# Kernel optimization log

Hardware: AMD Instinct MI355X
Metric: run time of the kernel (lower is better)

## Reference

```python
import jax, jax.numpy as jnp
import numpy as np

HIDDEN = 2048
INTER = 1408
NUM_EXPERTS = 8
TOP_K = 2
BATCH, SEQ = 2, 1024


def setup_inputs() -> dict:
    key = jax.random.key(0)
    ks = jax.random.split(key, 8)
    s = 0.02
    return {
        "x": jax.random.normal(ks[0], (BATCH, SEQ, HIDDEN), dtype=jnp.float32),
        "router_w": jax.random.normal(ks[1], (NUM_EXPERTS, HIDDEN), dtype=jnp.float32) * s,
        "gate_w": jax.random.normal(ks[2], (NUM_EXPERTS, INTER, HIDDEN), dtype=jnp.float32) * s,
        "up_w": jax.random.normal(ks[3], (NUM_EXPERTS, INTER, HIDDEN), dtype=jnp.float32) * s,
        "down_w": jax.random.normal(ks[4], (NUM_EXPERTS, HIDDEN, INTER), dtype=jnp.float32) * s,
        "shared_gate_w": jax.random.normal(ks[5], (INTER, HIDDEN), dtype=jnp.float32) * s,
        "shared_up_w": jax.random.normal(ks[6], (INTER, HIDDEN), dtype=jnp.float32) * s,
        "shared_down_w": jax.random.normal(ks[7], (HIDDEN, INTER), dtype=jnp.float32) * s,
    }


def reference(x, router_w, gate_w, up_w, down_w,
              shared_gate_w, shared_up_w, shared_down_w):
    B, S, H = x.shape
    T = B * S
    E = router_w.shape[0]
    xf = x.reshape(T, H)

    # Router: softmax over experts, top-k selection, renormalized weights
    logits = xf @ router_w.T                       # [T, E]
    probs = jax.nn.softmax(logits, axis=-1)
    topw, topi = jax.lax.top_k(probs, TOP_K)       # [T, K]
    topw = topw / jnp.sum(topw, axis=-1, keepdims=True)

    # Combine weight per (token, expert): scatter-add of top-k weights
    comb = jnp.zeros((T, E), dtype=xf.dtype).at[
        jnp.arange(T)[:, None], topi].add(topw)    # [T, E]

    # All-expert SwiGLU (grouped GEMM form of masked gather/MLP/scatter)
    g = jnp.einsum('th,eih->tei', xf, gate_w)      # [T, E, I]
    u = jnp.einsum('th,eih->tei', xf, up_w)
    hmid = jax.nn.silu(g) * u
    eo = jnp.einsum('tei,ehi->teh', hmid, down_w)  # [T, E, H]
    out = jnp.einsum('te,teh->th', comb, eo)       # weighted combine

    # Shared expert applied to every token
    sh = (jax.nn.silu(xf @ shared_gate_w.T) * (xf @ shared_up_w.T)) @ shared_down_w.T
    out = out + sh
    return out.reshape(B, S, H)
```

## Files before the change

kernel.cpp:

```cpp
#include <hip/hip_runtime.h>
#include <cstdint>
#include <cstddef>

#define T_TOK 2048
#define HID   2048
#define INTER 1408
#define NEXP  8
#define NPAIR 6144
#define SLICE 2883584
#define BKS   32

#define NI1   22
#define GP1   24
#define NB1   (9 * GP1 * 16)
#define NI2   32
#define GP2   32
#define NB2   (9 * GP2 * 16)

typedef __bf16 bf16x8 __attribute__((ext_vector_type(8)));
typedef float  floatx4 __attribute__((ext_vector_type(4)));

static const size_t XB_OFF   = 0;
static const size_t HM_OFF   = XB_OFF + (size_t)T_TOK * HID * 2;
static const size_t GB_OFF   = HM_OFF + (size_t)NPAIR * INTER * 2;
static const size_t UB_OFF   = GB_OFF + (size_t)9 * SLICE * 2;
static const size_t DB_OFF   = UB_OFF + (size_t)9 * SLICE * 2;
static const size_t TOK_OFF  = DB_OFF + (size_t)9 * SLICE * 2;
static const size_t WGT_OFF  = TOK_OFF + (size_t)NPAIR * 4;
static const size_t TE_OFF   = WGT_OFF + (size_t)NPAIR * 4;
static const size_t TW_OFF   = TE_OFF + (size_t)T_TOK * 2 * 4;
static const size_t CTRL_OFF = TW_OFF + (size_t)T_TOK * 2 * 4;

static __device__ __forceinline__ unsigned short f2bf(float f) {
    unsigned u = __float_as_uint(f);
    u += 0x7fffu + ((u >> 16) & 1u);
    return (unsigned short)(u >> 16);
}
static __device__ __forceinline__ unsigned pk2(float a, float b) {
    return (unsigned)f2bf(a) | ((unsigned)f2bf(b) << 16);
}
static __device__ __forceinline__ void g2l16(const void* g, void* l) {
    __builtin_amdgcn_global_load_lds(
        (const __attribute__((address_space(1))) unsigned int*)g,
        (__attribute__((address_space(3))) unsigned int*)l, 16, 0, 0);
}

__global__ __launch_bounds__(256) void k_cvt_x(const float* __restrict__ x,
                                               unsigned short* __restrict__ xb) {
    int gid = blockIdx.x * 256 + threadIdx.x;
    const float4* src = (const float4*)x;
    float4 a = src[gid * 2], b = src[gid * 2 + 1];
    uint4 o;
    o.x = pk2(a.x, a.y); o.y = pk2(a.z, a.w);
    o.z = pk2(b.x, b.y); o.w = pk2(b.z, b.w);
    ((uint4*)xb)[gid] = o;
}

__global__ __launch_bounds__(256) void k_cvt_w(const float* __restrict__ g,
                                               const float* __restrict__ u,
                                               const float* __restrict__ d,
                                               const float* __restrict__ sg,
                                               const float* __restrict__ su,
                                               const float* __restrict__ sd,
                                               unsigned short* __restrict__ gb,
                                               unsigned short* __restrict__ ub,
                                               unsigned short* __restrict__ db) {
    int sl = blockIdx.z;
    const float* src;
    unsigned short* dst;
    if (blockIdx.y == 0) {
        src = (sl < 8) ? g + (size_t)sl * SLICE : sg;
        dst = gb + (size_t)sl * SLICE;
    } else if (blockIdx.y == 1) {
        src = (sl < 8) ? u + (size_t)sl * SLICE : su;
        dst = ub + (size_t)sl * SLICE;
    } else {
        src = (sl < 8) ? d + (size_t)sl * SLICE : sd;
        dst = db + (size_t)sl * SLICE;
    }
    int gid = blockIdx.x * 256 + threadIdx.x;
    const float4* s4 = (const float4*)src;
    float4 a = s4[gid * 2], b = s4[gid * 2 + 1];
    uint4 o;
    o.x = pk2(a.x, a.y); o.y = pk2(a.z, a.w);
    o.z = pk2(b.x, b.y); o.w = pk2(b.z, b.w);
    ((uint4*)dst)[gid] = o;
}

__global__ __launch_bounds__(256) void k_router(const float* __restrict__ x,
                                                const float* __restrict__ rw,
                                                int* __restrict__ te, float* __restrict__ tw,
                                                int* __restrict__ counts) {
    int wave = threadIdx.x >> 6, lane = threadIdx.x & 63;
    int t = blockIdx.x * 4 + wave;
    const float* xp = x + (size_t)t * HID;

    float acc[8];
#pragma unroll
    for (int e = 0; e < 8; ++e) acc[e] = 0.f;
    for (int i = lane; i < HID; i += 64) {
        float xv = xp[i];
#pragma unroll
        for (int e = 0; e < 8; ++e) acc[e] = fmaf(xv, rw[e * HID + i], acc[e]);
    }
#pragma unroll
    for (int e = 0; e < 8; ++e) {
        float v = acc[e];
        for (int s = 32; s; s >>= 1) v += __shfl_xor(v, s, 64);
        acc[e] = v;
    }
    float mx = acc[0];
#pragma unroll
    for (int e = 1; e < 8; ++e) mx = fmaxf(mx, acc[e]);
    float p[8];
#pragma unroll
    for (int e = 0; e < 8; ++e) p[e] = __expf(acc[e] - mx);
    int i1 = 0; float v1 = p[0];
#pragma unroll
    for (int e = 1; e < 8; ++e) if (p[e] > v1) { v1 = p[e]; i1 = e; }
    int i2 = -1; float v2 = -1.f;
#pragma unroll
    for (int e = 0; e < 8; ++e) if (e != i1 && p[e] > v2) { v2 = p[e]; i2 = e; }
    float inv = 1.f / (v1 + v2);
    if (lane == 0) {
        te[2 * t] = i1;     tw[2 * t] = v1 * inv;
        te[2 * t + 1] = i2; tw[2 * t + 1] = v2 * inv;
        atomicAdd(&counts[i1], 1);
        atomicAdd(&counts[i2], 1);
    }
}

__global__ __launch_bounds__(256) void k_scatter(const int* __restrict__ te,
                                                 const float* __restrict__ tw,
                                                 int* __restrict__ ctrl,
                                                 int* __restrict__ tok, float* __restrict__ wgt) {
    __shared__ int soff[8];
    if (threadIdx.x < 8) {
        int s = 0;
        for (int e = 0; e < (int)threadIdx.x; ++e) s += ctrl[e];
        soff[threadIdx.x] = s;
    }
    __syncthreads();
    int t = blockIdx.x * 256 + threadIdx.x;
    if (t >= T_TOK) return;
#pragma unroll
    for (int k = 0; k < 2; ++k) {
        int e = te[2 * t + k];
        int slot = atomicAdd(&ctrl[8 + e], 1);
        int pp = soff[e] + slot;
        tok[pp] = t; wgt[pp] = tw[2 * t + k];
    }
    tok[2 * T_TOK + t] = t; wgt[2 * T_TOK + t] = 1.0f;
}

__global__ __launch_bounds__(256) void k_gemm1(const unsigned short* __restrict__ xb,
                                               const unsigned short* __restrict__ gwb,
                                               const unsigned short* __restrict__ uwb,
                                               const int* __restrict__ tok,
                                               const int* __restrict__ ctrl,
                                               unsigned short* __restrict__ hmid) {
    int h = blockIdx.x;
    int g8  = h & 7;
    int mt  = (h >> 3) & 15;
    int j   = h >> 7;
    int G   = j * 8 + g8;
    int e   = G / GP1;
    int bi  = G % GP1;
    if (bi >= NI1) return;
    int off = 0;
#pragma unroll
    for (int ee = 0; ee < 8; ++ee) if (ee < e) off += ctrl[ee];
    int cnt = (e < 8) ? ctrl[e] : T_TOK;
    int m0 = mt * 128;
    if (m0 >= cnt) return;
    int i0 = bi * 64;
    const unsigned short* gw = gwb + (size_t)e * SLICE;
    const unsigned short* uw = uwb + (size_t)e * SLICE;

    __shared__ __align__(16) unsigned short As[128 * BKS];
    __shared__ __align__(16) unsigned short Bg[64 * BKS];
    __shared__ __align__(16) unsigned short Bu[64 * BKS];

    int tid = threadIdx.x;
    int lane = tid & 63, wave = tid >> 6;
    int lr = lane >> 2, lc = (lane & 3) * 8;

    int r0 = m0 + wave * 32 + lr;
    int ap0 = off + r0;       if (ap0 > NPAIR - 1) ap0 = NPAIR - 1;
    int ap1 = off + r0 + 16;  if (ap1 > NPAIR - 1) ap1 = NPAIR - 1;
    const unsigned short* a0 = xb + (size_t)tok[ap0] * HID + lc;
    const unsigned short* a1 = xb + (size_t)tok[ap1] * HID + lc;
    const unsigned short* bg = gw + (size_t)(i0 + wave * 16 + lr) * HID + lc;
    const unsigned short* bu = uw + (size_t)(i0 + wave * 16 + lr) * HID + lc;

    unsigned short* lA0 = &As[(wave * 32) * BKS];
    unsigned short* lA1 = &As[(wave * 32 + 16) * BKS];
    unsigned short* lBg = &Bg[(wave * 16) * BKS];
    unsigned short* lBu = &Bu[(wave * 16) * BKS];

    floatx4 accg[2][4], accu[2][4];
#pragma unroll
    for (int mi = 0; mi < 2; ++mi)
#pragma unroll
        for (int ni = 0; ni < 4; ++ni) {
            accg[mi][ni] = (floatx4){0.f, 0.f, 0.f, 0.f};
            accu[mi][ni] = (floatx4){0.f, 0.f, 0.f, 0.f};
        }

    int wm = wave * 32;
    int mrow = lane & 15, kq = (lane >> 4) * 8;

    for (int kt = 0; kt < HID / BKS; ++kt) {
        int k0 = kt * BKS;
        g2l16(a0 + k0, lA0);
        g2l16(a1 + k0, lA1);
        g2l16(bg + k0, lBg);
        g2l16(bu + k0, lBu);
        __syncthreads();

        bf16x8 af0 = *(const bf16x8*)&As[(wm + mrow) * BKS + kq];
        bf16x8 af1 = *(const bf16x8*)&As[(wm + 16 + mrow) * BKS + kq];
#pragma unroll
        for (int ni = 0; ni < 4; ++ni) {
            bf16x8 bgv = *(const bf16x8*)&Bg[(ni * 16 + mrow) * BKS + kq];
            bf16x8 buv = *(const bf16x8*)&Bu[(ni * 16 + mrow) * BKS + kq];
            accg[0][ni] = __builtin_amdgcn_mfma_f32_16x16x32_bf16(af0, bgv, accg[0][ni], 0, 0, 0);
            accu[0][ni] = __builtin_amdgcn_mfma_f32_16x16x32_bf16(af0, buv, accu[0][ni], 0, 0, 0);
            accg[1][ni] = __builtin_amdgcn_mfma_f32_16x16x32_bf16(af1, bgv, accg[1][ni], 0, 0, 0);
            accu[1][ni] = __builtin_amdgcn_mfma_f32_16x16x32_bf16(af1, buv, accu[1][ni], 0, 0, 0);
        }
        __syncthreads();
    }

    int quad = lane >> 4, col = lane & 15;
#pragma unroll
    for (int mi = 0; mi < 2; ++mi)
#pragma unroll
        for (int ni = 0; ni < 4; ++ni)
#pragma unroll
            for (int r = 0; r < 4; ++r) {
                int row = m0 + wm + mi * 16 + quad * 4 + r;
                if (row < cnt) {
                    float g = accg[mi][ni][r], u = accu[mi][ni][r];
                    float s = g / (1.f + __expf(-g));
                    hmid[(size_t)(off + row) * INTER + i0 + ni * 16 + col] = f2bf(s * u);
                }
            }
}

__global__ __launch_bounds__(256) void k_gemm2(const unsigned short* __restrict__ hmid,
                                               const unsigned short* __restrict__ dwb,
                                               const int* __restrict__ tok,
                                               const float* __restrict__ wgt,
                                               const int* __restrict__ ctrl,
                                               float* __restrict__ out) {
    int h = blockIdx.x;
    int g8  = h & 7;
    int mt  = (h >> 3) & 15;
    int j   = h >> 7;
    int G   = j * 8 + g8;
    int e   = G / GP2;
    int bn  = G % GP2;
    int off = 0;
#pragma unroll
    for (int ee = 0; ee < 8; ++ee) if (ee < e) off += ctrl[ee];
    int cnt = (e < 8) ? ctrl[e] : T_TOK;
    int m0 = mt * 128;
    if (m0 >= cnt) return;
    int n0 = bn * 64;
    const unsigned short* dw = dwb + (size_t)e * SLICE;

    __shared__ __align__(16) unsigned short As[128 * BKS];
    __shared__ __align__(16) unsigned short Bd[64 * BKS];

    int tid = threadIdx.x;
    int lane = tid & 63, wave = tid >> 6;
    int lr = lane >> 2, lc = (lane & 3) * 8;

    int r0 = m0 + wave * 32 + lr;
    int ap0 = off + r0;       if (ap0 > NPAIR - 1) ap0 = NPAIR - 1;
    int ap1 = off + r0 + 16;  if (ap1 > NPAIR - 1) ap1 = NPAIR - 1;
    const unsigned short* a0 = hmid + (size_t)ap0 * INTER + lc;
    const unsigned short* a1 = hmid + (size_t)ap1 * INTER + lc;
    const unsigned short* bd = dw + (size_t)(n0 + wave * 16 + lr) * INTER + lc;

    unsigned short* lA0 = &As[(wave * 32) * BKS];
    unsigned short* lA1 = &As[(wave * 32 + 16) * BKS];
    unsigned short* lBd = &Bd[(wave * 16) * BKS];

    floatx4 acc[2][4];
#pragma unroll
    for (int mi = 0; mi < 2; ++mi)
#pragma unroll
        for (int ni = 0; ni < 4; ++ni) acc[mi][ni] = (floatx4){0.f, 0.f, 0.f, 0.f};

    int wm = wave * 32;
    int mrow = lane & 15, kq = (lane >> 4) * 8;

    for (int kt = 0; kt < INTER / BKS; ++kt) {
        int k0 = kt * BKS;
        g2l16(a0 + k0, lA0);
        g2l16(a1 + k0, lA1);
        g2l16(bd + k0, lBd);
        __syncthreads();

        bf16x8 af0 = *(const bf16x8*)&As[(wm + mrow) * BKS + kq];
        bf16x8 af1 = *(const bf16x8*)&As[(wm + 16 + mrow) * BKS + kq];
#pragma unroll
        for (int ni = 0; ni < 4; ++ni) {
            bf16x8 bv = *(const bf16x8*)&Bd[(ni * 16 + mrow) * BKS + kq];
            acc[0][ni] = __builtin_amdgcn_mfma_f32_16x16x32_bf16(af0, bv, acc[0][ni], 0, 0, 0);
            acc[1][ni] = __builtin_amdgcn_mfma_f32_16x16x32_bf16(af1, bv, acc[1][ni], 0, 0, 0);
        }
        __syncthreads();
    }

    int quad = lane >> 4, col = lane & 15;
#pragma unroll
    for (int mi = 0; mi < 2; ++mi)
#pragma unroll
        for (int r = 0; r < 4; ++r) {
            int row = m0 + wm + mi * 16 + quad * 4 + r;
            if (row < cnt) {
                int p = off + row;
                int t = tok[p];
                float w = wgt[p];
#pragma unroll
                for (int ni = 0; ni < 4; ++ni)
                    atomicAdd(&out[(size_t)t * HID + n0 + ni * 16 + col], w * acc[mi][ni][r]);
            }
        }
}

extern "C" void kernel_launch(void* const* d_in, const int* in_sizes, int n_in,
                              void* d_out, int out_size, void* d_ws, size_t ws_size,
                              hipStream_t stream) {
    const float* x        = (const float*)d_in[0];
    const float* router_w = (const float*)d_in[1];
    const float* gate_w   = (const float*)d_in[2];
    const float* up_w     = (const float*)d_in[3];
    const float* down_w   = (const float*)d_in[4];
    const float* sgate    = (const float*)d_in[5];
    const float* sup      = (const float*)d_in[6];
    const float* sdown    = (const float*)d_in[7];
    float* out = (float*)d_out;

    char* ws = (char*)d_ws;
    unsigned short* xb   = (unsigned short*)(ws + XB_OFF);
    unsigned short* hmid = (unsigned short*)(ws + HM_OFF);
    unsigned short* gwb  = (unsigned short*)(ws + GB_OFF);
    unsigned short* uwb  = (unsigned short*)(ws + UB_OFF);
    unsigned short* dwb  = (unsigned short*)(ws + DB_OFF);
    int*   tok  = (int*)(ws + TOK_OFF);
    float* wgt  = (float*)(ws + WGT_OFF);
    int*   te   = (int*)(ws + TE_OFF);
    float* tw   = (float*)(ws + TW_OFF);
    int*   ctrl = (int*)(ws + CTRL_OFF);

    hipMemsetAsync(ctrl, 0, 16 * sizeof(int), stream);
    hipMemsetAsync(out, 0, (size_t)T_TOK * HID * sizeof(float), stream);

    k_cvt_x  <<<(T_TOK * HID) / 8 / 256, 256, 0, stream>>>(x, xb);
    k_cvt_w  <<<dim3(SLICE / 8 / 256, 3, 9), 256, 0, stream>>>(gate_w, up_w, down_w,
                                                               sgate, sup, sdown, gwb, uwb, dwb);
    k_router <<<T_TOK / 4, 256, 0, stream>>>(x, router_w, te, tw, ctrl);
    k_scatter<<<T_TOK / 256, 256, 0, stream>>>(te, tw, ctrl, tok, wgt);

    k_gemm1<<<NB1, 256, 0, stream>>>(xb, gwb, uwb, tok, ctrl, hmid);
    k_gemm2<<<NB2, 256, 0, stream>>>(hmid, dwb, tok, wgt, ctrl, out);
}
```

Before: 668.5 us.

## Add device-side scheduler to balance grouped-GEMM tiles across XCDs

Result: slower. 766.0 us (+14.6%).

```diff
diff --git a/kernel.cpp b/kernel.cpp
--- a/kernel.cpp
+++ b/kernel.cpp
@@ -11,11 +11,22 @@
 #define BKS   32
 
 #define NI1   22
-#define GP1   24
-#define NB1   (9 * GP1 * 16)
 #define NI2   32
-#define GP2   32
-#define NB2   (9 * GP2 * 16)
+#define NG1   (9 * NI1)
+#define NG2   (9 * NI2)
+#define CAP1  176
+#define CAP2  240
+#define NB1   (8 * CAP1)
+#define NB2   (8 * CAP2)
+
+#define C_CNT  0
+#define C_FILL 8
+#define C_OFFS 16
+#define C_N1   25
+#define C_N2   33
+#define C_S1   48
+#define C_S2   (48 + NB1)
+#define C_TOT  (C_S2 + NB2)
 
 typedef __bf16 bf16x8 __attribute__((ext_vector_type(8)));
 typedef float  floatx4 __attribute__((ext_vector_type(4)));
@@ -130,6 +141,57 @@
     }
 }
 
+__global__ __launch_bounds__(64) void k_sched(int* __restrict__ ctrl) {
+    __shared__ int asg1[NG1], asg2[NG2];
+    int lane = threadIdx.x;
+    if (lane == 0) {
+        int s = 0;
+        for (int e = 0; e < 8; ++e) { ctrl[C_OFFS + e] = s; s += ctrl[C_CNT + e]; }
+        ctrl[C_OFFS + 8] = s;
+        int m[9];
+        for (int e = 0; e < 8; ++e) m[e] = (ctrl[C_CNT + e] + 127) >> 7;
+        m[8] = 16;
+        int load[8], n[8];
+        for (int q = 0; q < 8; ++q) { load[q] = 0; n[q] = 0; }
+        for (int gi = 0; gi < NG1; ++gi) {
+            int e = (gi < NI1) ? 8 : (gi - NI1) / NI1;
+            int w = m[e];
+            int x = 0;
+            for (int q = 1; q < 8; ++q) if (load[q] < load[x]) x = q;
+            asg1[gi] = x | (n[x] << 4);
+            load[x] += w; n[x] += w;
+        }
+        for (int q = 0; q < 8; ++q) ctrl[C_N1 + q] = n[q];
+        for (int q = 0; q < 8; ++q) { load[q] = 0; n[q] = 0; }
+        for (int gi = 0; gi < NG2; ++gi) {
+            int e = (gi < NI2) ? 8 : (gi - NI2) / NI2;
+            int w = m[e];
+            int x = 0;
+            for (int q = 1; q < 8; ++q) if (load[q] < load[x]) x = q;
+            asg2[gi] = x | (n[x] << 4);
+            load[x] += w; n[x] += w;
+        }
+        for (int q = 0; q < 8; ++q) ctrl[C_N2 + q] = n[q];
+    }
+    __syncthreads();
+    for (int gi = lane; gi < NG1; gi += 64) {
+        int e  = (gi < NI1) ? 8 : (gi - NI1) / NI1;
+        int bi = (gi < NI1) ? gi : (gi - NI1) % NI1;
+        int w  = (e < 8) ? ((ctrl[C_CNT + e] + 127) >> 7) : 16;
+        int a = asg1[gi], x = a & 15, base = a >> 4;
+        for (int mt = 0; mt < w; ++mt)
+            ctrl[C_S1 + x + 8 * (base + mt)] = (e << 16) | (bi << 8) | mt;
+    }
+    for (int gi = lane; gi < NG2; gi += 64) {
+        int e  = (gi < NI2) ? 8 : (gi - NI2) / NI2;
+        int bn = (gi < NI2) ? gi : (gi - NI2) % NI2;
+        int w  = (e < 8) ? ((ctrl[C_CNT + e] + 127) >> 7) : 16;
+        int a = asg2[gi], x = a & 15, base = a >> 4;
+        for (int mt = 0; mt < w; ++mt)
+            ctrl[C_S2 + x + 8 * (base + mt)] = (e << 16) | (bn << 8) | mt;
+    }
+}
+
 __global__ __launch_bounds__(256) void k_scatter(const int* __restrict__ te,
                                                  const float* __restrict__ tw,
                                                  int* __restrict__ ctrl,
@@ -146,7 +208,7 @@
 #pragma unroll
     for (int k = 0; k < 2; ++k) {
         int e = te[2 * t + k];
-        int slot = atomicAdd(&ctrl[8 + e], 1);
+        int slot = atomicAdd(&ctrl[C_FILL + e], 1);
         int pp = soff[e] + slot;
         tok[pp] = t; wgt[pp] = tw[2 * t + k];
     }
@@ -159,20 +221,13 @@
                                                const int* __restrict__ tok,
                                                const int* __restrict__ ctrl,
                                                unsigned short* __restrict__ hmid) {
-    int h = blockIdx.x;
-    int g8  = h & 7;
-    int mt  = (h >> 3) & 15;
-    int j   = h >> 7;
-    int G   = j * 8 + g8;
-    int e   = G / GP1;
-    int bi  = G % GP1;
-    if (bi >= NI1) return;
-    int off = 0;
-#pragma unroll
-    for (int ee = 0; ee < 8; ++ee) if (ee < e) off += ctrl[ee];
-    int cnt = (e < 8) ? ctrl[e] : T_TOK;
+    int x = blockIdx.x & 7, idx = blockIdx.x >> 3;
+    if (idx >= ctrl[C_N1 + x]) return;
+    int wrd = ctrl[C_S1 + x + 8 * idx];
+    int e = wrd >> 16, bi = (wrd >> 8) & 255, mt = wrd & 255;
+    int off = ctrl[C_OFFS + e];
+    int cnt = (e < 8) ? ctrl[C_CNT + e] : T_TOK;
     int m0 = mt * 128;
-    if (m0 >= cnt) return;
     int i0 = bi * 64;
     const unsigned short* gw = gwb + (size_t)e * SLICE;
     const unsigned short* uw = uwb + (size_t)e * SLICE;
@@ -254,19 +309,13 @@
                                                const float* __restrict__ wgt,
                                                const int* __restrict__ ctrl,
                                                float* __restrict__ out) {
-    int h = blockIdx.x;
-    int g8  = h & 7;
-    int mt  = (h >> 3) & 15;
-    int j   = h >> 7;
-    int G   = j * 8 + g8;
-    int e   = G / GP2;
-    int bn  = G % GP2;
-    int off = 0;
-#pragma unroll
-    for (int ee = 0; ee < 8; ++ee) if (ee < e) off += ctrl[ee];
-    int cnt = (e < 8) ? ctrl[e] : T_TOK;
+    int x = blockIdx.x & 7, idx = blockIdx.x >> 3;
+    if (idx >= ctrl[C_N2 + x]) return;
+    int wrd = ctrl[C_S2 + x + 8 * idx];
+    int e = wrd >> 16, bn = (wrd >> 8) & 255, mt = wrd & 255;
+    int off = ctrl[C_OFFS + e];
+    int cnt = (e < 8) ? ctrl[C_CNT + e] : T_TOK;
     int m0 = mt * 128;
-    if (m0 >= cnt) return;
     int n0 = bn * 64;
     const unsigned short* dw = dwb + (size_t)e * SLICE;
 
@@ -364,6 +413,7 @@
     k_cvt_w  <<<dim3(SLICE / 8 / 256, 3, 9), 256, 0, stream>>>(gate_w, up_w, down_w,
                                                                sgate, sup, sdown, gwb, uwb, dwb);
     k_router <<<T_TOK / 4, 256, 0, stream>>>(x, router_w, te, tw, ctrl);
+    k_sched  <<<1, 64, 0, stream>>>(ctrl);
     k_scatter<<<T_TOK / 256, 256, 0, stream>>>(te, tw, ctrl, tok, wgt);
 
     k_gemm1<<<NB1, 256, 0, stream>>>(xb, gwb, uwb, tok, ctrl, hmid);
```
